# Performance work log

Hardware: AMD Instinct MI355X
Metric: run time of the kernel (lower is better)

The kernel has to match this reference:

```python
import jax, jax.numpy as jnp
import numpy as np

RANK = 8
ALPHA = 16.0
SCALING = ALPHA / RANK


def setup_inputs() -> dict:
    key = jax.random.key(0)
    ks = jax.random.split(key, 13)
    T, B, D = 8, 1024, 1024
    H1, H2, H3 = 2048, 2048, 1024
    r = RANK
    def n(k, shape, scale):
        return jax.random.normal(k, shape, dtype=jnp.float32) * scale
    return {
        "x": n(ks[0], (T, B, D), 1.0),
        "k0": n(ks[1], (D, H1), D ** -0.5),
        "b0": n(ks[2], (H1,), 0.02),
        "d0": n(ks[3], (D, r, T), D ** -0.5),
        "u0": n(ks[4], (r, H1, T), 0.02),  # zeros-init in original; random for nontrivial test
        "k1": n(ks[5], (H1, H2), H1 ** -0.5),
        "b1": n(ks[6], (H2,), 0.02),
        "d1": n(ks[7], (H1, r, T), H1 ** -0.5),
        "u1": n(ks[8], (r, H2, T), 0.02),
        "k2": n(ks[9], (H2, H3), H2 ** -0.5),
        "b2": n(ks[10], (H3,), 0.02),
        "d2": n(ks[11], (H2, r, T), H2 ** -0.5),
        "u2": n(ks[12], (r, H3, T), 0.02),
    }


def _lora_dense(h, k, b, d, u):
    # frozen base matmul: [t,b,i] @ [i,f] -> [t,b,f]
    base = jnp.einsum('tbi,if->tbf', h, k) + b
    # per-task low-rank adapter: down [i,r,t], up [r,f,t]
    delta = jnp.einsum('tbi,irt,rft->tbf', h, d, u) * SCALING
    return base + delta


def reference(x, k0, b0, d0, u0, k1, b1, d1, u1, k2, b2, d2, u2):
    h = jax.nn.relu(_lora_dense(x, k0, b0, d0, u0))
    h = jax.nn.relu(_lora_dense(h, k1, b1, d1, u1))
    h = _lora_dense(h, k2, b2, d2, u2)  # no activation on final layer
    return h
```

## Files before the change

### kernel.cpp

```cpp
#include <hip/hip_runtime.h>

typedef unsigned short u16;
typedef __attribute__((ext_vector_type(8))) __bf16 bf16x8;
typedef __attribute__((ext_vector_type(8))) unsigned short u16x8;
typedef __attribute__((ext_vector_type(4))) float f32x4;

__device__ __forceinline__ float bf2f(u16 h) {
    return __uint_as_float(((unsigned int)h) << 16);
}
__device__ __forceinline__ u16 f2bf(float f) {
    unsigned int u = __float_as_uint(f);
    u += 0x7fffu + ((u >> 16) & 1u);
    return (u16)(u >> 16);
}
__device__ __forceinline__ bf16x8 zero_bf16x8() {
    union { unsigned int u[4]; bf16x8 v; } z;
    z.u[0] = z.u[1] = z.u[2] = z.u[3] = 0u;
    return z.v;
}
__device__ __forceinline__ void gload_lds16(const void* g, void* l) {
    __builtin_amdgcn_global_load_lds(
        (const __attribute__((address_space(1))) unsigned int*)g,
        (__attribute__((address_space(3))) unsigned int*)l, 16, 0, 0);
}
__device__ __forceinline__ void store_out(u16* p, float v)  { *p = f2bf(v); }
__device__ __forceinline__ void store_out(float* p, float v){ *p = v; }


__device__ __forceinline__ void do_cvt(
    const float* __restrict__ in, u16* __restrict__ out, int blk)
{
    int i = (blk * 256 + (int)threadIdx.x) * 8;
    float4 a = *(const float4*)(in + i);
    float4 b = *(const float4*)(in + i + 4);
    u16x8 o;
    o[0] = f2bf(a.x); o[1] = f2bf(a.y); o[2] = f2bf(a.z); o[3] = f2bf(a.w);
    o[4] = f2bf(b.x); o[5] = f2bf(b.y); o[6] = f2bf(b.z); o[7] = f2bf(b.w);
    *(u16x8*)(out + i) = o;
}

__device__ __forceinline__ void do_transpose(
    const float* __restrict__ in, u16* __restrict__ out, int K, int F, int t)
{
    __shared__ u16 tt[32][33];
    int fb = t % (F >> 5), kb = t / (F >> 5);
    int f0 = fb << 5, k0 = kb << 5;
    int lx = threadIdx.x & 31;
    int ly = threadIdx.x >> 5;
#pragma unroll
    for (int i = 0; i < 4; ++i) {
        int k = ly + i * 8;
        tt[k][lx] = f2bf(in[(size_t)(k0 + k) * F + f0 + lx]);
    }
    __syncthreads();
#pragma unroll
    for (int i = 0; i < 4; ++i) {
        int fy = ly + i * 8;
        out[(size_t)(f0 + fy) * K + k0 + lx] = tt[lx][fy];
    }
}

__device__ __forceinline__ void do_prep_d(
    const float* __restrict__ d, u16* __restrict__ o, int K, int blk)
{
    int i = blk * 256 + (int)threadIdx.x;
    int r = i & 7;
    int k = (i >> 3) % K;
    int t = i / (K * 8);
    o[i] = f2bf(d[((size_t)k * 8 + r) * 8 + t]);
}

__device__ __forceinline__ void do_prep_u(
    const float* __restrict__ u, u16* __restrict__ o, int F, int blk)
{
    int i = blk * 256 + (int)threadIdx.x;
    int r = i & 7;
    int f = (i >> 3) % F;
    int t = i / (F * 8);
    o[i] = f2bf(u[((size_t)r * F + f) * 8 + t] * 2.0f);
}

__global__ __launch_bounds__(256) void prep_all(
    const float* x, const float* k0, const float* k1, const float* k2,
    const float* d0, const float* d1, const float* d2,
    const float* u0, const float* u1, const float* u2,
    u16* xb, u16* k0T, u16* k1T, u16* k2T,
    u16* dS0, u16* dS1, u16* dS2, u16* uS0, u16* uS1, u16* uS2)
{
    int b = blockIdx.x;
    if      (b < 4096)  do_cvt(x, xb, b);
    else if (b < 6144)  do_transpose(k0, k0T, 1024, 2048, b - 4096);
    else if (b < 10240) do_transpose(k1, k1T, 2048, 2048, b - 6144);
    else if (b < 12288) do_transpose(k2, k2T, 2048, 1024, b - 10240);
    else if (b < 12544) do_prep_d(d0, dS0, 1024, b - 12288);
    else if (b < 13056) do_prep_d(d1, dS1, 2048, b - 12544);
    else if (b < 13568) do_prep_d(d2, dS2, 2048, b - 13056);
    else if (b < 14080) do_prep_u(u0, uS0, 2048, b - 13568);
    else if (b < 14592) do_prep_u(u1, uS1, 2048, b - 14080);
    else                do_prep_u(u2, uS2, 1024, b - 14592);
}

__global__ __launch_bounds__(256) void lora_down(
    const u16* __restrict__ H, const u16* __restrict__ dS,
    u16* __restrict__ Aout, int K)
{
    int gt   = blockIdx.x * 256 + threadIdx.x;
    int row  = gt >> 3;
    int oct  = gt & 7;
    int task = row >> 10;
    const u16* hrow = H  + (size_t)row * K;
    const u16* dt   = dS + (size_t)task * K * 8;
    float acc[8];
#pragma unroll
    for (int r = 0; r < 8; ++r) acc[r] = 0.f;
    int kpt  = K >> 3;
    int kbeg = oct * kpt;
    for (int kk = kbeg; kk < kbeg + kpt; kk += 8) {
        u16x8 h8 = *(const u16x8*)(hrow + kk);
#pragma unroll
        for (int j = 0; j < 8; ++j) {
            float hv = bf2f(h8[j]);
            u16x8 dv = *(const u16x8*)(dt + (size_t)(kk + j) * 8);
#pragma unroll
            for (int r = 0; r < 8; ++r)
                acc[r] += hv * bf2f(dv[r]);
        }
    }
#pragma unroll
    for (int r = 0; r < 8; ++r) {
        acc[r] += __shfl_xor(acc[r], 1);
        acc[r] += __shfl_xor(acc[r], 2);
        acc[r] += __shfl_xor(acc[r], 4);
    }
    if (oct == 0) {
        u16x8 o;
#pragma unroll
        for (int r = 0; r < 8; ++r) o[r] = f2bf(acc[r]);
        *(u16x8*)(Aout + (size_t)row * 8) = o;
    }
}


#define WVMC do { if constexpr (SAL + SBL == 4) { \
                    asm volatile("s_waitcnt vmcnt(4)" ::: "memory"); \
                  } else if constexpr (SAL + SBL == 3) { \
                    asm volatile("s_waitcnt vmcnt(3)" ::: "memory"); \
                  } else { \
                    asm volatile("s_waitcnt vmcnt(2)" ::: "memory"); } } while (0)
#define WVMP do { if constexpr (SAL == 2) { \
                    asm volatile("s_waitcnt vmcnt(2)" ::: "memory"); \
                  } else { \
                    asm volatile("s_waitcnt vmcnt(1)" ::: "memory"); } } while (0)
#define WVM0  asm volatile("s_waitcnt vmcnt(0)" ::: "memory")
#define PHASE_END do { __builtin_amdgcn_sched_barrier(0); \
                       __builtin_amdgcn_s_barrier(); } while (0)

#define DS_A(c, mh) do { \
    _Pragma("unroll") for (int mm = 0; mm < NMH; ++mm) \
    _Pragma("unroll") for (int ks = 0; ks < 2; ++ks) \
        aF[mm][ks] = *(const bf16x8*)((const char*)&sA[c][0] + \
                       arowb + ((mh)*NMH+mm)*4096 + (ks ? cb1 : cb0)); } while (0)

#define DS_B(c, nh, bset) do { \
    _Pragma("unroll") for (int nn = 0; nn < NBH; ++nn) \
    _Pragma("unroll") for (int ks = 0; ks < 2; ++ks) \
        bset[nn][ks] = *(const bf16x8*)((const char*)&sB[c][0] + \
                       browb + ((nh)*NBH+nn)*8192 + (ks ? cb1 : cb0)); } while (0)

#define MFMAQ(mh, nh, bset) do { \
    _Pragma("unroll") for (int ks = 0; ks < 2; ++ks) \
    _Pragma("unroll") for (int mm = 0; mm < NMH; ++mm) \
    _Pragma("unroll") for (int nn = 0; nn < NBH; ++nn) \
        acc[(mh)*NMH+mm][(nh)*NBH+nn] = __builtin_amdgcn_mfma_f32_16x16x32_bf16( \
            aF[mm][ks], bset[nn][ks], acc[(mh)*NMH+mm][(nh)*NBH+nn], 0, 0, 0); } while (0)

#define STAGE_A(c, h, kt) do { \
    _Pragma("unroll") for (int s = 0; s < SAL; ++s) \
        gload_lds16((const char*)A + (size_t)(unsigned)(aBase + \
                      ((h)*BMH + s*64)*(K*2) + (kt)*128), \
                    (char*)&sA[c][0] + (h)*(BMH*128) + s*8192 + tdst); } while (0)

#define STAGE_B(c, h, kt) do { \
    _Pragma("unroll") for (int s = 0; s < SBL; ++s) \
        gload_lds16((const char*)BT + (size_t)(unsigned)(bBase + \
                      ((h)*BNH + s*64)*(K*2) + (kt)*128), \
                    (char*)&sB[c][0] + (h)*(BNH*128) + s*8192 + tdst); } while (0)

template<int RELU, int BM, int BN, int WPEU, typename OUT_T>
__global__ __launch_bounds__(512, WPEU) void gemm_lora8(
    const u16* __restrict__ A, const u16* __restrict__ BT,
    const u16* __restrict__ ALR, const u16* __restrict__ US,
    const float* __restrict__ bias, OUT_T* __restrict__ C,
    int N, int K)
{
    constexpr int SAL = BM / 128;
    constexpr int SBL = BN / 128;
    constexpr int NMH = BM / 64;
    constexpr int NMB = BM / 32;
    constexpr int NBH = BN / 128;
    constexpr int NBN = BN / 64;
    constexpr int BMH = BM / 2;
    constexpr int BNH = BN / 2;

    __shared__ __align__(16) u16 sA[2][BM * 64];
    __shared__ __align__(16) u16 sB[2][BN * 64];

    const int tid  = threadIdx.x;
    const int lane = tid & 63;
    const int wave = tid >> 6;
    const int wr   = wave >> 2;
    const int wc   = wave & 3;
    const int l15  = lane & 15;
    const int lg   = lane >> 4;

    const int nwg = gridDim.x;
    const int orig = blockIdx.x;
    const int q = nwg >> 3, r = nwg & 7;
    const int x = orig & 7, o = orig >> 3;
    const int wg = (x < r ? x * (q + 1) : r * (q + 1) + (x - r) * q) + o;
    const int nbn  = N / BN;
    const int bm   = wg / nbn;
    const int bn   = wg % nbn;
    const int brow = bm * BM;
    const int bcol = bn * BN;
    const int task = brow >> 10;

    const int trow = tid >> 3;
    const int tkc  = (tid & 7) ^ (trow & 7);
    const int tdst = tid * 16;
    const int aBase = (brow + trow) * (K * 2) + tkc * 16;
    const int bBase = (bcol + trow) * (K * 2) + tkc * 16;

    const int rp    = l15 & 7;
    const int cb0   = ((lg ^ (rp & 3)) << 4) | ((rp & 4) << 4);
    const int cb1   = cb0 ^ 64;
    const int arowb = (wr * 16 + l15) * 128;
    const int browb = (wc * 16 + l15) * 128;

    f32x4 acc[NMB][NBN];
    const f32x4 zf = {0.f, 0.f, 0.f, 0.f};
#pragma unroll
    for (int m = 0; m < NMB; ++m)
#pragma unroll
        for (int n = 0; n < NBN; ++n) acc[m][n] = zf;

    bf16x8 aF[NMH][2], bF0[NBH][2], bF1[NBH][2];

    STAGE_A(0, 0, 0); STAGE_B(0, 0, 0); STAGE_A(0, 1, 0); STAGE_B(0, 1, 0);
    STAGE_A(1, 0, 1); STAGE_B(1, 0, 1);
    WVMC;
    PHASE_END;
    DS_A(0, 0); DS_B(0, 0, bF0);

    const int iters = K >> 7;
#pragma unroll 1
    for (int i = 0; i < iters; ++i) {
        const int t1 = 2 * i + 1, t2 = 2 * i + 2, t3 = 2 * i + 3;
        const bool nl = (i + 1 < iters);

        STAGE_A(1, 1, t1);
        MFMAQ(0, 0, bF0);
        DS_B(0, 1, bF1);
        PHASE_END;
        STAGE_B(1, 1, t1);
        MFMAQ(0, 1, bF1);
        DS_A(0, 1);
        PHASE_END;
        if (nl) STAGE_A(0, 0, t2);
        MFMAQ(1, 0, bF0);
        if (nl) { WVMP; } else { WVM0; }
        PHASE_END;
        if (nl) STAGE_B(0, 0, t2);
        MFMAQ(1, 1, bF1);
        DS_A(1, 0); DS_B(1, 0, bF0);
        PHASE_END;
        if (nl) STAGE_A(0, 1, t2);
        MFMAQ(0, 0, bF0);
        DS_B(1, 1, bF1);
        PHASE_END;
        if (nl) STAGE_B(0, 1, t2);
        MFMAQ(0, 1, bF1);
        DS_A(1, 1);
        PHASE_END;
        if (nl) STAGE_A(1, 0, t3);
        MFMAQ(1, 0, bF0);
        if (nl) { WVMP; }
        PHASE_END;
        if (nl) STAGE_B(1, 0, t3);
        MFMAQ(1, 1, bF1);
        if (nl) { DS_A(0, 0); DS_B(0, 0, bF0); }
        PHASE_END;
    }

    bf16x8 z8 = zero_bf16x8();
    bf16x8 bU[NBN];
#pragma unroll
    for (int n = 0; n < NBN; ++n) {
        int col = bcol + n * 64 + wc * 16 + l15;
        bU[n] = (lg == 0) ? *(const bf16x8*)(US + ((size_t)task * N + col) * 8) : z8;
    }
#pragma unroll
    for (int m = 0; m < NMB; ++m) {
        int row = brow + m * 32 + wr * 16 + l15;
        bf16x8 aL = (lg == 0) ? *(const bf16x8*)(ALR + (size_t)row * 8) : z8;
#pragma unroll
        for (int n = 0; n < NBN; ++n)
            acc[m][n] = __builtin_amdgcn_mfma_f32_16x16x32_bf16(
                aL, bU[n], acc[m][n], 0, 0, 0);
    }

#pragma unroll
    for (int n = 0; n < NBN; ++n) {
        int col  = bcol + n * 64 + wc * 16 + l15;
        float bv = bias[col];
#pragma unroll
        for (int m = 0; m < NMB; ++m) {
            int row0 = brow + m * 32 + wr * 16 + lg * 4;
#pragma unroll
            for (int rr = 0; rr < 4; ++rr) {
                float v = acc[m][n][rr] + bv;
                if (RELU) v = fmaxf(v, 0.0f);
                store_out(&C[(size_t)(row0 + rr) * N + col], v);
            }
        }
    }
}


extern "C" void kernel_launch(void* const* d_in, const int* in_sizes, int n_in,
                              void* d_out, int out_size, void* d_ws, size_t ws_size,
                              hipStream_t stream) {
    const float* x  = (const float*)d_in[0];
    const float* k0 = (const float*)d_in[1];
    const float* b0 = (const float*)d_in[2];
    const float* d0 = (const float*)d_in[3];
    const float* u0 = (const float*)d_in[4];
    const float* k1 = (const float*)d_in[5];
    const float* b1 = (const float*)d_in[6];
    const float* d1 = (const float*)d_in[7];
    const float* u1 = (const float*)d_in[8];
    const float* k2 = (const float*)d_in[9];
    const float* b2 = (const float*)d_in[10];
    const float* d2 = (const float*)d_in[11];
    const float* u2 = (const float*)d_in[12];

    const int T = 8, B = 1024, D = 1024, H1 = 2048, H2 = 2048, H3 = 1024;
    const int M = T * B;

    u16* w = (u16*)d_ws;
    size_t off = 0;
    u16* xb  = w + off; off += (size_t)M * D;
    u16* k0T = w + off; off += (size_t)H1 * D;
    u16* k1T = w + off; off += (size_t)H2 * H1;
    u16* k2T = w + off; off += (size_t)H3 * H2;
    u16* dS0 = w + off; off += (size_t)T * D * 8;
    u16* dS1 = w + off; off += (size_t)T * H1 * 8;
    u16* dS2 = w + off; off += (size_t)T * H2 * 8;
    u16* uS0 = w + off; off += (size_t)T * H1 * 8;
    u16* uS1 = w + off; off += (size_t)T * H2 * 8;
    u16* uS2 = w + off; off += (size_t)T * H3 * 8;
    u16* h1  = w + off; off += (size_t)M * H1;
    u16* h2  = w + off; off += (size_t)M * H2;
    u16* Ab  = w + off; off += (size_t)M * 8;
    (void)ws_size; (void)in_sizes; (void)n_in; (void)out_size;

    prep_all<<<14848, 256, 0, stream>>>(
        x, k0, k1, k2, d0, d1, d2, u0, u1, u2,
        xb, k0T, k1T, k2T, dS0, dS1, dS2, uS0, uS1, uS2);

    lora_down<<<(M * 8) / 256, 256, 0, stream>>>(xb, dS0, Ab, D);
    gemm_lora8<1, 256, 256, 2, u16><<<(M / 256) * (H1 / 256), 512, 0, stream>>>(
        xb, k0T, Ab, uS0, b0, h1, H1, D);
    lora_down<<<(M * 8) / 256, 256, 0, stream>>>(h1, dS1, Ab, H1);
    gemm_lora8<1, 256, 256, 2, u16><<<(M / 256) * (H2 / 256), 512, 0, stream>>>(
        h1, k1T, Ab, uS1, b1, h2, H2, H1);
    lora_down<<<(M * 8) / 256, 256, 0, stream>>>(h2, dS2, Ab, H2);
    gemm_lora8<0, 128, 128, 4, float><<<(M / 128) * (H3 / 128), 512, 0, stream>>>(
        h2, k2T, Ab, uS2, b2, (float*)d_out, H3, H2);
}
```

Before: 258.9 us.

## Fuse first LoRA-down into prep kernel and add pipelined 128x256 GEMM for last layer

Computes the layer-0 LoRA down-projection directly from the fp32 input and d0 inside the prep kernel as extra blocks, which removes one separate kernel launch. It also adds a new GEMM kernel for the final layer. That kernel uses a 128x256 tile with two LDS buffers and an interleaved schedule of async global-to-LDS loads, LDS reads and MFMA phases, gated by explicit vmcnt waits. The down-projection reads d0 with a strided, uncoalesced pattern. The hand-written wait counts are fragile and could break correctness if the schedule is off.

```diff
diff --git a/kernel.cpp b/kernel.cpp
--- a/kernel.cpp
+++ b/kernel.cpp
@@ -80,12 +80,51 @@
     o[i] = f2bf(u[((size_t)r * F + f) * 8 + t] * 2.0f);
 }
 
+__device__ __forceinline__ void do_lora0(
+    const float* __restrict__ x, const float* __restrict__ d0,
+    u16* __restrict__ Ab, int blk)
+{
+    int gt   = blk * 256 + (int)threadIdx.x;
+    int row  = gt >> 3;
+    int oct  = gt & 7;
+    int task = row >> 10;
+    const float4* xr = (const float4*)(x + (size_t)row * 1024);
+    float acc[8];
+#pragma unroll
+    for (int r = 0; r < 8; ++r) acc[r] = 0.f;
+    for (int c = oct * 32; c < oct * 32 + 32; ++c) {
+        float4 xv = xr[c];
+        int k0 = c * 4;
+#pragma unroll
+        for (int j = 0; j < 4; ++j) {
+            float xs = (&xv.x)[j];
+            const float* dk = d0 + ((size_t)(k0 + j) * 8) * 8 + task;
+#pragma unroll
+            for (int r = 0; r < 8; ++r)
+                acc[r] += xs * dk[r * 8];
+        }
+    }
+#pragma unroll
+    for (int r = 0; r < 8; ++r) {
+        acc[r] += __shfl_xor(acc[r], 1);
+        acc[r] += __shfl_xor(acc[r], 2);
+        acc[r] += __shfl_xor(acc[r], 4);
+    }
+    if (oct == 0) {
+        u16x8 o;
+#pragma unroll
+        for (int r = 0; r < 8; ++r) o[r] = f2bf(acc[r]);
+        *(u16x8*)(Ab + (size_t)row * 8) = o;
+    }
+}
+
 __global__ __launch_bounds__(256) void prep_all(
     const float* x, const float* k0, const float* k1, const float* k2,
     const float* d0, const float* d1, const float* d2,
     const float* u0, const float* u1, const float* u2,
     u16* xb, u16* k0T, u16* k1T, u16* k2T,
-    u16* dS0, u16* dS1, u16* dS2, u16* uS0, u16* uS1, u16* uS2)
+    u16* dS0, u16* dS1, u16* dS2, u16* uS0, u16* uS1, u16* uS2,
+    u16* Ab)
 {
     int b = blockIdx.x;
     if      (b < 4096)  do_cvt(x, xb, b);
@@ -97,7 +136,8 @@
     else if (b < 13568) do_prep_d(d2, dS2, 2048, b - 13056);
     else if (b < 14080) do_prep_u(u0, uS0, 2048, b - 13568);
     else if (b < 14592) do_prep_u(u1, uS1, 2048, b - 14080);
-    else                do_prep_u(u2, uS2, 1024, b - 14592);
+    else if (b < 14848) do_prep_u(u2, uS2, 1024, b - 14592);
+    else                do_lora0(x, d0, Ab, b - 14848);
 }
 
 __global__ __launch_bounds__(256) void lora_down(
@@ -315,6 +355,171 @@
         float bv = bias[col];
 #pragma unroll
         for (int m = 0; m < NMB; ++m) {
+            int row0 = brow + m * 32 + wr * 16 + lg * 4;
+#pragma unroll
+            for (int rr = 0; rr < 4; ++rr) {
+                float v = acc[m][n][rr] + bv;
+                if (RELU) v = fmaxf(v, 0.0f);
+                store_out(&C[(size_t)(row0 + rr) * N + col], v);
+            }
+        }
+    }
+}
+
+
+#define PVM3 asm volatile("s_waitcnt vmcnt(3)" ::: "memory")
+#define PVM1 asm volatile("s_waitcnt vmcnt(1)" ::: "memory")
+#define PVM0 asm volatile("s_waitcnt vmcnt(0)" ::: "memory")
+
+#define PDS_A(dst, c, mh) do { \
+    _Pragma("unroll") for (int mm = 0; mm < 2; ++mm) \
+    _Pragma("unroll") for (int ks = 0; ks < 2; ++ks) \
+        dst[mm][ks] = *(const bf16x8*)((const char*)&sA[c][0] + \
+                       arowb + ((mh)*2+mm)*4096 + (ks ? cb1 : cb0)); } while (0)
+
+#define PDS_B(dst, c, nh) do { \
+    _Pragma("unroll") for (int nn = 0; nn < 2; ++nn) \
+    _Pragma("unroll") for (int ks = 0; ks < 2; ++ks) \
+        dst[nn][ks] = *(const bf16x8*)((const char*)&sB[c][0] + \
+                       browb + ((nh)*2+nn)*8192 + (ks ? cb1 : cb0)); } while (0)
+
+#define PMFMAQ(aset, bset, mh, nh) do { \
+    _Pragma("unroll") for (int ks = 0; ks < 2; ++ks) \
+    _Pragma("unroll") for (int mm = 0; mm < 2; ++mm) \
+    _Pragma("unroll") for (int nn = 0; nn < 2; ++nn) \
+        acc[(mh)*2+mm][(nh)*2+nn] = __builtin_amdgcn_mfma_f32_16x16x32_bf16( \
+            aset[mm][ks], bset[nn][ks], acc[(mh)*2+mm][(nh)*2+nn], 0, 0, 0); } while (0)
+
+#define PSTAGE_A(c, h, kt) do { \
+        gload_lds16((const char*)A + (size_t)(unsigned)(aBase + \
+                      ((h)*64)*(K*2) + (kt)*128), \
+                    (char*)&sA[c][0] + (h)*8192 + tdst); } while (0)
+
+#define PSTAGE_B(c, h, kt) do { \
+    _Pragma("unroll") for (int s = 0; s < 2; ++s) \
+        gload_lds16((const char*)BT + (size_t)(unsigned)(bBase + \
+                      ((h)*128 + s*64)*(K*2) + (kt)*128), \
+                    (char*)&sB[c][0] + (h)*16384 + s*8192 + tdst); } while (0)
+
+template<int RELU, typename OUT_T>
+__global__ __launch_bounds__(512, 2) void gemm_lorap(
+    const u16* __restrict__ A, const u16* __restrict__ BT,
+    const u16* __restrict__ ALR, const u16* __restrict__ US,
+    const float* __restrict__ bias, OUT_T* __restrict__ C,
+    int N, int K)
+{
+    __shared__ __align__(16) u16 sA[2][128 * 64];
+    __shared__ __align__(16) u16 sB[2][256 * 64];
+
+    const int tid  = threadIdx.x;
+    const int lane = tid & 63;
+    const int wave = tid >> 6;
+    const int wr   = wave >> 2;
+    const int wc   = wave & 3;
+    const int l15  = lane & 15;
+    const int lg   = lane >> 4;
+
+    const int nwg = gridDim.x;
+    const int orig = blockIdx.x;
+    const int q = nwg >> 3, r = nwg & 7;
+    const int x = orig & 7, o = orig >> 3;
+    const int wg = (x < r ? x * (q + 1) : r * (q + 1) + (x - r) * q) + o;
+    const int nbn  = N >> 8;
+    const int bm   = wg / nbn;
+    const int bn   = wg % nbn;
+    const int brow = bm << 7;
+    const int bcol = bn << 8;
+    const int task = brow >> 10;
+
+    const int trow = tid >> 3;
+    const int tkc  = (tid & 7) ^ (trow & 7);
+    const int tdst = tid * 16;
+    const int aBase = (brow + trow) * (K * 2) + tkc * 16;
+    const int bBase = (bcol + trow) * (K * 2) + tkc * 16;
+
+    const int rp    = l15 & 7;
+    const int cb0   = ((lg ^ (rp & 3)) << 4) | ((rp & 4) << 4);
+    const int cb1   = cb0 ^ 64;
+    const int arowb = (wr * 16 + l15) * 128;
+    const int browb = (wc * 16 + l15) * 128;
+
+    f32x4 acc[4][4];
+    const f32x4 zf = {0.f, 0.f, 0.f, 0.f};
+#pragma unroll
+    for (int m = 0; m < 4; ++m)
+#pragma unroll
+        for (int n = 0; n < 4; ++n) acc[m][n] = zf;
+
+    bf16x8 aFa[2][2], aFb[2][2], bF0[2][2], bF1[2][2];
+
+    PSTAGE_A(0, 0, 0); PSTAGE_B(0, 0, 0); PSTAGE_A(0, 1, 0); PSTAGE_B(0, 1, 0);
+    PSTAGE_A(1, 0, 1); PSTAGE_B(1, 0, 1);
+    PVM3;
+    PHASE_END;
+    PDS_A(aFa, 0, 0); PDS_B(bF0, 0, 0);
+
+    const int iters = K >> 7;
+#pragma unroll 1
+    for (int i = 0; i < iters; ++i) {
+        const int t1 = 2 * i + 1, t2 = 2 * i + 2, t3 = 2 * i + 3;
+        const bool nl = (i + 1 < iters);
+
+        PDS_B(bF1, 0, 1);
+        PSTAGE_A(1, 1, t1);
+        PMFMAQ(aFa, bF0, 0, 0);
+        PHASE_END;
+        PDS_A(aFb, 0, 1);
+        PSTAGE_B(1, 1, t1);
+        PMFMAQ(aFa, bF1, 0, 1);
+        PHASE_END;
+        if (nl) PSTAGE_A(0, 0, t2);
+        PMFMAQ(aFb, bF0, 1, 0);
+        if (nl) { PVM1; } else { PVM0; }
+        PHASE_END;
+        PDS_A(aFa, 1, 0); PDS_B(bF0, 1, 0);
+        if (nl) PSTAGE_B(0, 0, t2);
+        PMFMAQ(aFb, bF1, 1, 1);
+        PHASE_END;
+        PDS_B(bF1, 1, 1);
+        if (nl) PSTAGE_A(0, 1, t2);
+        PMFMAQ(aFa, bF0, 0, 0);
+        PHASE_END;
+        PDS_A(aFb, 1, 1);
+        if (nl) PSTAGE_B(0, 1, t2);
+        PMFMAQ(aFa, bF1, 0, 1);
+        PHASE_END;
+        if (nl) PSTAGE_A(1, 0, t3);
+        PMFMAQ(aFb, bF0, 1, 0);
+        if (nl) { PVM1; }
+        PHASE_END;
+        if (nl) { PDS_A(aFa, 0, 0); PDS_B(bF0, 0, 0); PSTAGE_B(1, 0, t3); }
+        PMFMAQ(aFb, bF1, 1, 1);
+        PHASE_END;
+    }
+
+    bf16x8 z8 = zero_bf16x8();
+    bf16x8 bU[4];
+#pragma unroll
+    for (int n = 0; n < 4; ++n) {
+        int col = bcol + n * 64 + wc * 16 + l15;
+        bU[n] = (lg == 0) ? *(const bf16x8*)(US + ((size_t)task * N + col) * 8) : z8;
+    }
+#pragma unroll
+    for (int m = 0; m < 4; ++m) {
+        int row = brow + m * 32 + wr * 16 + l15;
+        bf16x8 aL = (lg == 0) ? *(const bf16x8*)(ALR + (size_t)row * 8) : z8;
+#pragma unroll
+        for (int n = 0; n < 4; ++n)
+            acc[m][n] = __builtin_amdgcn_mfma_f32_16x16x32_bf16(
+                aL, bU[n], acc[m][n], 0, 0, 0);
+    }
+
+#pragma unroll
+    for (int n = 0; n < 4; ++n) {
+        int col  = bcol + n * 64 + wc * 16 + l15;
+        float bv = bias[col];
+#pragma unroll
+        for (int m = 0; m < 4; ++m) {
             int row0 = brow + m * 32 + wr * 16 + lg * 4;
 #pragma unroll
             for (int rr = 0; rr < 4; ++rr) {
@@ -364,17 +569,16 @@
     u16* Ab  = w + off; off += (size_t)M * 8;
     (void)ws_size; (void)in_sizes; (void)n_in; (void)out_size;
 
-    prep_all<<<14848, 256, 0, stream>>>(
+    prep_all<<<15104, 256, 0, stream>>>(
         x, k0, k1, k2, d0, d1, d2, u0, u1, u2,
-        xb, k0T, k1T, k2T, dS0, dS1, dS2, uS0, uS1, uS2);
-
-    lora_down<<<(M * 8) / 256, 256, 0, stream>>>(xb, dS0, Ab, D);
+        xb, k0T, k1T, k2T, dS0, dS1, dS2, uS0, uS1, uS2, Ab);
+
     gemm_lora8<1, 256, 256, 2, u16><<<(M / 256) * (H1 / 256), 512, 0, stream>>>(
         xb, k0T, Ab, uS0, b0, h1, H1, D);
     lora_down<<<(M * 8) / 256, 256, 0, stream>>>(h1, dS1, Ab, H1);
     gemm_lora8<1, 256, 256, 2, u16><<<(M / 256) * (H2 / 256), 512, 0, stream>>>(
         h1, k1T, Ab, uS1, b1, h2, H2, H1);
     lora_down<<<(M * 8) / 256, 256, 0, stream>>>(h2, dS2, Ab, H2);
-    gemm_lora8<0, 128, 128, 4, float><<<(M / 128) * (H3 / 128), 512, 0, stream>>>(
+    gemm_lorap<0, float><<<(M / 128) * (H3 / 256), 512, 0, stream>>>(
         h2, k2T, Ab, uS2, b2, (float*)d_out, H3, H2);
 }
```

Measured after the change: 554.3 us. +114.1%, slower.
